# Kernel tuning notes

Measured on AMD Instinct MI355X. Metric: run time of the kernel, lower is better.

The kernel has to match this reference:

```python
import jax, jax.numpy as jnp
import numpy as np

B, S, E, H, M, N_BLOCKS, V = 32, 32, 512, 8, 2, 4, 10000
START = 0

def _pos_encoding(s_len, e_dim):
    # Standard sinusoidal positional encoding (base 10000), as in the repo's PositionalEncoding.
    pos = np.arange(s_len)[:, None].astype(np.float32)
    div = np.exp(np.arange(0, e_dim, 2).astype(np.float32) * (-np.log(10000.0) / e_dim))
    pe = np.zeros((s_len, e_dim), dtype=np.float32)
    pe[:, 0::2] = np.sin(pos * div)
    pe[:, 1::2] = np.cos(pos * div)
    return jnp.asarray(pe)

def _ln(x, g, b, eps=1e-5):
    mu = x.mean(-1, keepdims=True)
    var = ((x - mu) ** 2).mean(-1, keepdims=True)
    return g * (x - mu) / jnp.sqrt(var + eps) + b

def _mha(q_in, kv_in, Wq, Wk, Wv, Wo, bq, bk, bv, bo):
    b_, tq, e = q_in.shape
    dh = e // H
    q = (q_in @ Wq + bq).reshape(b_, tq, H, dh)
    k = (kv_in @ Wk + bk).reshape(b_, -1, H, dh)
    v = (kv_in @ Wv + bv).reshape(b_, -1, H, dh)
    att = jax.nn.softmax(jnp.einsum('bqhd,bkhd->bhqk', q, k) * (1.0 / np.sqrt(dh)), axis=-1)
    out = jnp.einsum('bhqk,bkhd->bqhd', att, v).reshape(b_, tq, e)
    return out @ Wo + bo

def setup_inputs():
    key = jax.random.key(0)
    ks = jax.random.split(key, 8)
    s = 0.02
    return {
        'noise': jax.random.uniform(ks[0], (B, S), dtype=jnp.float32),
        'W_in': jax.random.normal(ks[1], (M, S, S), dtype=jnp.float32) * s,
        'b_in': jnp.zeros((M, S), dtype=jnp.float32),
        'emb': jax.random.normal(ks[2], (V, E), dtype=jnp.float32) * s,
        'Wsa': jax.random.normal(ks[3], (N_BLOCKS, 4, E, E), dtype=jnp.float32) * s,
        'bsa': jnp.zeros((N_BLOCKS, 4, E), dtype=jnp.float32),
        'Wca': jax.random.normal(ks[4], (N_BLOCKS, 4, E, E), dtype=jnp.float32) * s,
        'bca': jnp.zeros((N_BLOCKS, 4, E), dtype=jnp.float32),
        'Wff': jax.random.normal(ks[5], (N_BLOCKS, 2, E, E), dtype=jnp.float32) * s,
        'bff': jnp.zeros((N_BLOCKS, 2, E), dtype=jnp.float32),
        'ln_g': jnp.ones((N_BLOCKS, 3, E), dtype=jnp.float32),
        'ln_b': jnp.zeros((N_BLOCKS, 3, E), dtype=jnp.float32),
        'soft_W': jax.random.normal(ks[6], (E, V), dtype=jnp.float32) * s,
        'soft_b': jnp.zeros((V,), dtype=jnp.float32),
    }

def reference(noise, W_in, b_in, emb, Wsa, bsa, Wca, bca, Wff, bff, ln_g, ln_b, soft_W, soft_b):
    pe = _pos_encoding(S, E)  # [S, E]
    # inEmb2: M stacked Linear(S, S) applied to the latent noise vector
    w = noise
    for m in range(M):
        w = w @ W_in[m] + b_in[m]
    # unsqueeze(-1).repeat(1,1,E): broadcast the scalar per position across the embedding dim
    w = jnp.broadcast_to(w[:, :, None], (B, S, E))
    # <START> token embedding + positional encoding of position 0
    Y = jnp.broadcast_to(emb[START], (B, 1, E)) + pe[0:1]
    out_sent = [jnp.broadcast_to(jax.nn.one_hot(START, V, dtype=jnp.float32), (B, V))]
    for tok in range(1, S):
        output = Y  # [B, tok, E]
        wt = w[:, :tok]
        for n in range(N_BLOCKS):
            h = _ln(output + _mha(output, output, Wsa[n, 0], Wsa[n, 1], Wsa[n, 2], Wsa[n, 3], bsa[n, 0], bsa[n, 1], bsa[n, 2], bsa[n, 3]), ln_g[n, 0], ln_b[n, 0])
            h = _ln(h + _mha(h, wt, Wca[n, 0], Wca[n, 1], Wca[n, 2], Wca[n, 3], bca[n, 0], bca[n, 1], bca[n, 2], bca[n, 3]), ln_g[n, 1], ln_b[n, 1])
            ff = jax.nn.relu(h @ Wff[n, 0] + bff[n, 0]) @ Wff[n, 1] + bff[n, 1]
            output = _ln(h + ff, ln_g[n, 2], ln_b[n, 2])
        out_tok = output[:, tok - 1]                       # [B, E]
        probs = jax.nn.softmax(out_tok @ soft_W + soft_b)  # [B, V]
        out_sent.append(probs)
        ids = jnp.argmax(probs, axis=-1)                   # greedy token
        nxt = emb[ids] + pe[tok]                           # embed + add posenc (Y[:, tok] += posEnc[:, tok])
        Y = jnp.concatenate([Y, nxt[:, None]], axis=1)
    return jnp.stack(out_sent, axis=1)  # [B, S, V]
```

## Files before the change

### kernel.cpp

```cpp
#include <hip/hip_runtime.h>
#include <cmath>

constexpr int kB = 32, kS = 32, kE = 512, kH = 8, kV = 10000, kNB = 4;
constexpr int kQ = 3 * kE;
constexpr int ROWS = 4;
constexpr int TT = 1024;

__device__ float g_w[kB * kS];
__device__ float g_pe[kS * kE];
__device__ float g_Y[kB * kS * kE];
__device__ float g_qkvbuf[kNB][kB * kS * kQ];
__device__ float g_actb[kNB][kB * kS * kE];
__device__ float g_logits[kB * kV];
__device__ float g_U[kNB * kE * kH];
__device__ float g_a0[kNB * kH];
__device__ float g_G[kNB * kH * kE];
__device__ float g_c0[kNB * kE];
__device__ float g_ck[kNB * kE];
__device__ float g_cv[kNB * kE];

__global__ void onehot_k(float* __restrict__ out) {
    int i = blockIdx.x * 256 + threadIdx.x;
    if (i >= kB * kV) return;
    int b = i / kV, v = i - b * kV;
    out[(size_t)b * kS * kV + v] = (v == 0) ? 1.f : 0.f;
}

__global__ void pe_k(float* __restrict__ pe) {
    int i = blockIdx.x * 256 + threadIdx.x;
    int s = i >> 9, e = i & 511;
    int base = e & ~1;
    float div = expf((float)base * (-logf(10000.f) / (float)kE));
    float ang = (float)s * div;
    pe[i] = (e & 1) ? cosf(ang) : sinf(ang);
}

__global__ void compute_w_k(const float* __restrict__ noise, const float* __restrict__ W_in,
                            const float* __restrict__ b_in, float* __restrict__ w) {
    __shared__ float X[kB * kS], T[kB * kS];
    int tid = threadIdx.x;
    X[tid] = noise[tid];
    __syncthreads();
    int r = tid >> 5, c = tid & 31;
    float acc = b_in[c];
    for (int k = 0; k < 32; ++k) acc = fmaf(X[r * 32 + k], W_in[k * 32 + c], acc);
    T[tid] = acc;
    __syncthreads();
    acc = b_in[32 + c];
    for (int k = 0; k < 32; ++k) acc = fmaf(T[r * 32 + k], W_in[1024 + k * 32 + c], acc);
    w[tid] = acc;
}

__global__ __launch_bounds__(256) void initY_k(const float* __restrict__ emb,
                                               const float* __restrict__ pe,
                                               float* __restrict__ Y,
                                               const float* __restrict__ Wq0,
                                               const float* __restrict__ bq0,
                                               float* __restrict__ qkv0) {
    __shared__ float ys[kE];
    int b = blockIdx.x, tid = threadIdx.x;
    for (int j = tid; j < kE; j += 256) {
        float v = emb[j] + pe[j];
        Y[(size_t)(b * kS) * kE + j] = v;
        ys[j] = v;
    }
    __syncthreads();
#pragma unroll
    for (int m = 0; m < 6; ++m) {
        int j = tid + 256 * m;
        const float* Wc = Wq0 + (size_t)(j >> 9) * (kE * kE) + (j & 511);
        float acc = bq0[j];
        for (int k = 0; k < kE; ++k) acc = fmaf(ys[k], Wc[(size_t)k * kE], acc);
        qkv0[(size_t)(b * kS) * kQ + j] = acc;
    }
}

__global__ __launch_bounds__(256) void colsum_k(const float* __restrict__ Wca,
                                                float* __restrict__ ck, float* __restrict__ cv) {
    int n = blockIdx.x, q = blockIdx.y;
    const float* Wk = Wca + (size_t)n * 4 * kE * kE + kE * kE;
    const float* Wv = Wk + kE * kE;
    __shared__ float p1[2][128], p2[2][128];
    int jj = threadIdx.x & 127, half = threadIdx.x >> 7;
    int j = q * 128 + jj;
    float s1 = 0.f, s2 = 0.f;
    for (int e = half * 256; e < half * 256 + 256; ++e) {
        s1 += Wk[(size_t)e * kE + j];
        s2 += Wv[(size_t)e * kE + j];
    }
    p1[half][jj] = s1; p2[half][jj] = s2;
    __syncthreads();
    if (half == 0) {
        ck[n * kE + j] = p1[0][jj] + p1[1][jj];
        cv[n * kE + j] = p2[0][jj] + p2[1][jj];
    }
}

__global__ __launch_bounds__(256) void precross2_k(const float* __restrict__ Wca,
                                                   const float* __restrict__ bca,
                                                   const float* __restrict__ ck,
                                                   const float* __restrict__ cv,
                                                   float* __restrict__ U, float* __restrict__ a0,
                                                   float* __restrict__ G, float* __restrict__ c0) {
    int n = blockIdx.x, s = blockIdx.y;
    const float* Wq = Wca + (size_t)n * 4 * kE * kE;
    const float* Wo = Wq + 3 * kE * kE;
    const float* bq = bca + n * 4 * kE;
    const float* bv = bq + 2 * kE;
    const float* bo = bq + 3 * kE;
    __shared__ float cks[kE], cvs[kE];
    __shared__ float cred[2][128];
    int tid = threadIdx.x;
    for (int p = tid; p < kE; p += 256) { cks[p] = ck[n * kE + p]; cvs[p] = cv[n * kE + p]; }
    __syncthreads();
    for (int p = tid; p < 128 * kH; p += 256) {
        int e = s * 128 + (p >> 3), h = p & 7;
        float acc = 0.f;
        for (int d = 0; d < 64; ++d) acc = fmaf(Wq[(size_t)e * kE + h * 64 + d], cks[h * 64 + d], acc);
        U[n * kE * kH + e * kH + h] = acc;
    }
    for (int p = tid; p < kH * 128; p += 256) {
        int h = p >> 7, j = s * 128 + (p & 127);
        float acc = 0.f;
        for (int d = 0; d < 64; ++d) acc = fmaf(cvs[h * 64 + d], Wo[(size_t)(h * 64 + d) * kE + j], acc);
        G[n * kH * kE + h * kE + j] = acc;
    }
    {
        int jj = tid & 127, half = tid >> 7;
        int j = s * 128 + jj;
        float acc = 0.f;
        for (int e = half * 256; e < half * 256 + 256; ++e) acc = fmaf(bv[e], Wo[(size_t)e * kE + j], acc);
        cred[half][jj] = acc;
        __syncthreads();
        if (half == 0) c0[n * kE + j] = bo[j] + cred[0][jj] + cred[1][jj];
    }
    if (s == 0 && tid < kH) {
        float acc = 0.f;
        for (int d = 0; d < 64; ++d) acc = fmaf(bq[tid * 64 + d], cks[tid * 64 + d], acc);
        a0[n * kH + tid] = acc;
    }
}

__device__ __forceinline__ void rowsum4_1024(float v[ROWS], float (*red)[ROWS], float out[ROWS]) {
    int lane = threadIdx.x & 63, w = threadIdx.x >> 6;
#pragma unroll
    for (int i = 0; i < ROWS; ++i) {
        float s = v[i];
#pragma unroll
        for (int o = 32; o > 0; o >>= 1) s += __shfl_xor(s, o);
        v[i] = s;
    }
    if (lane == 0) {
#pragma unroll
        for (int i = 0; i < ROWS; ++i) red[w][i] = v[i];
    }
    __syncthreads();
#pragma unroll
    for (int i = 0; i < ROWS; ++i) {
        float s = 0.f;
#pragma unroll
        for (int w2 = 0; w2 < 16; ++w2) s += red[w2][i];
        out[i] = s;
    }
    __syncthreads();
}

__device__ __forceinline__ void ln4_1024(float val[ROWS], const float* __restrict__ g,
                                         const float* __restrict__ bb, float (*red)[ROWS], int j,
                                         bool act) {
    float s[ROWS], mean[ROWS], var[ROWS];
#pragma unroll
    for (int i = 0; i < ROWS; ++i) s[i] = act ? val[i] : 0.f;
    rowsum4_1024(s, red, mean);
#pragma unroll
    for (int i = 0; i < ROWS; ++i) {
        mean[i] *= (1.f / (float)kE);
        if (act) val[i] -= mean[i];
        s[i] = act ? val[i] * val[i] : 0.f;
    }
    rowsum4_1024(s, red, var);
#pragma unroll
    for (int i = 0; i < ROWS; ++i) {
        float rstd = rsqrtf(var[i] * (1.f / (float)kE) + 1e-5f);
        if (act) val[i] = g[j] * val[i] * rstd + bb[j];
    }
}

__device__ __forceinline__ void gemm_phase4(const float (*in)[kE], const float* __restrict__ W,
                                            float (*out)[kE], int kg, int jt) {
    float acc[ROWS][4];
#pragma unroll
    for (int i = 0; i < ROWS; ++i)
#pragma unroll
        for (int c = 0; c < 4; ++c) acc[i][c] = 0.f;
    const int kbase = kg * 64;
    const int j4 = jt * 4;
#pragma unroll 8
    for (int kk = 0; kk < 64; kk += 4) {
        float4 av[ROWS];
#pragma unroll
        for (int i = 0; i < ROWS; ++i) av[i] = *(const float4*)(&in[i][kbase + kk]);
        const float* Wr = W + (size_t)(kbase + kk) * kE + j4;
        const float4 w0 = *(const float4*)(Wr);
        const float4 w1 = *(const float4*)(Wr + kE);
        const float4 w2 = *(const float4*)(Wr + 2 * kE);
        const float4 w3 = *(const float4*)(Wr + 3 * kE);
#pragma unroll
        for (int i = 0; i < ROWS; ++i) {
            acc[i][0] = fmaf(av[i].x, w0.x, acc[i][0]);
            acc[i][0] = fmaf(av[i].y, w1.x, acc[i][0]);
            acc[i][0] = fmaf(av[i].z, w2.x, acc[i][0]);
            acc[i][0] = fmaf(av[i].w, w3.x, acc[i][0]);
            acc[i][1] = fmaf(av[i].x, w0.y, acc[i][1]);
            acc[i][1] = fmaf(av[i].y, w1.y, acc[i][1]);
            acc[i][1] = fmaf(av[i].z, w2.y, acc[i][1]);
            acc[i][1] = fmaf(av[i].w, w3.y, acc[i][1]);
            acc[i][2] = fmaf(av[i].x, w0.z, acc[i][2]);
            acc[i][2] = fmaf(av[i].y, w1.z, acc[i][2]);
            acc[i][2] = fmaf(av[i].z, w2.z, acc[i][2]);
            acc[i][2] = fmaf(av[i].w, w3.z, acc[i][2]);
            acc[i][3] = fmaf(av[i].x, w0.w, acc[i][3]);
            acc[i][3] = fmaf(av[i].y, w1.w, acc[i][3]);
            acc[i][3] = fmaf(av[i].z, w2.w, acc[i][3]);
            acc[i][3] = fmaf(av[i].w, w3.w, acc[i][3]);
        }
    }
    if (kg == 0) {
#pragma unroll
        for (int i = 0; i < ROWS; ++i)
            *(float4*)(&out[i][j4]) = make_float4(acc[i][0], acc[i][1], acc[i][2], acc[i][3]);
    }
    __syncthreads();
#pragma unroll
    for (int r = 1; r < 8; ++r) {
        if (kg == r) {
#pragma unroll
            for (int i = 0; i < ROWS; ++i) {
                float4 c = *(float4*)(&out[i][j4]);
                c.x += acc[i][0]; c.y += acc[i][1]; c.z += acc[i][2]; c.w += acc[i][3];
                *(float4*)(&out[i][j4]) = c;
            }
        }
        __syncthreads();
    }
}

__global__ __launch_bounds__(1024) void tail4w_k(
    const float* __restrict__ qkv_cur, const float* __restrict__ in_res,
    const float* __restrict__ Wo, const float* __restrict__ bo,
    const float* __restrict__ g0, const float* __restrict__ lb0,
    const float* __restrict__ Um, const float* __restrict__ a0m,
    const float* __restrict__ Gm, const float* __restrict__ c0m,
    const float* __restrict__ g1, const float* __restrict__ lb1,
    const float* __restrict__ W1, const float* __restrict__ fb1,
    const float* __restrict__ W2, const float* __restrict__ fb2,
    const float* __restrict__ g2, const float* __restrict__ lb2,
    const float* __restrict__ wvec, float* __restrict__ act_out,
    const float* __restrict__ Wqn, const float* __restrict__ bqn,
    float* __restrict__ qkv_next, int t, int r0_off) {
    __shared__ float bufA[ROWS][kE];
    __shared__ float bufC[ROWS][kE];
    __shared__ float Us[kE * kH];
    __shared__ float att_s[16][kS];
    __shared__ float alp[ROWS][kH][4];
    __shared__ float om_s[ROWS][kH];
    __shared__ float w_s[kS];
    __shared__ float red[16][ROWS];

    const int b = blockIdx.x;
    const int r0 = r0_off + blockIdx.y * ROWS;
    const int tid = threadIdx.x;
    const int lane = tid & 63, wid = tid >> 6;
    const int kg = tid >> 7, jt = tid & 127;
    const bool act = (tid < kE);
    int rr[ROWS]; bool valid[ROWS];
#pragma unroll
    for (int i = 0; i < ROWS; ++i) {
        int r = r0 + i;
        valid[i] = (r < t);
        rr[i] = valid[i] ? r : (t - 1);
    }

    for (int p = tid; p < ROWS * kE; p += TT) {
        int i = p >> 9, d = p & 511;
        bufA[i][d] = qkv_cur[(size_t)(b * kS + rr[i]) * kQ + d];
    }
    for (int p = tid; p < kE * kH; p += TT) Us[p] = Um[p];
    if (tid < t) w_s[tid] = wvec[b * kS + tid];
    __syncthreads();

    {
        const int i = wid & 3;
        const int hb = (wid >> 2) * 2;
#pragma unroll
        for (int hh = 0; hh < 2; ++hh) {
            const int h = hb + hh;
            float sc = -3.0e38f;
            if (lane < t) {
                const float* Kr = qkv_cur + (size_t)(b * kS + lane) * kQ + kE + h * 64;
                float a = 0.f;
#pragma unroll
                for (int d4 = 0; d4 < 16; ++d4) {
                    const float4 kv = *(const float4*)(Kr + d4 * 4);
                    const float4 qv = *(const float4*)(&bufA[i][h * 64 + d4 * 4]);
                    a = fmaf(qv.x, kv.x, a); a = fmaf(qv.y, kv.y, a);
                    a = fmaf(qv.z, kv.z, a); a = fmaf(qv.w, kv.w, a);
                }
                sc = a * 0.125f;
            }
            float m = sc;
#pragma unroll
            for (int o = 32; o > 0; o >>= 1) m = fmaxf(m, __shfl_xor(m, o));
            float e = (lane < t) ? expf(sc - m) : 0.f;
            float ss = e;
#pragma unroll
            for (int o = 32; o > 0; o >>= 1) ss += __shfl_xor(ss, o);
            if (lane < t) att_s[wid][lane] = e / ss;
            float acc = 0.f;
            const float* Vb = qkv_cur + (size_t)(b * kS) * kQ + 2 * kE + h * 64 + lane;
            for (int k = 0; k < t; ++k) acc = fmaf(att_s[wid][k], Vb[(size_t)k * kQ], acc);
            bufA[i][h * 64 + lane] = acc;
        }
    }
    __syncthreads();

    float val[ROWS], hreg[ROWS], h2reg[ROWS];

    float resv[ROWS];
#pragma unroll
    for (int i = 0; i < ROWS; ++i)
        resv[i] = act ? in_res[(size_t)(b * kS + rr[i]) * kE + tid] : 0.f;
    gemm_phase4(bufA, Wo, bufC, kg, jt);
    {
        float btid = act ? bo[tid] : 0.f;
#pragma unroll
        for (int i = 0; i < ROWS; ++i) val[i] = act ? (bufC[i][tid] + btid + resv[i]) : 0.f;
        ln4_1024(val, g0, lb0, red, act ? tid : 0, act);
#pragma unroll
        for (int i = 0; i < ROWS; ++i) {
            hreg[i] = val[i];
            if (act) bufA[i][tid] = val[i];
        }
    }
    __syncthreads();

    if (tid < ROWS * kH * 4) {
        int i = tid >> 5, h = (tid >> 2) & 7, cs = tid & 3;
        float a = 0.f;
        for (int e = cs * 128; e < cs * 128 + 128; ++e) a = fmaf(bufA[i][e], Us[e * kH + h], a);
        alp[i][h][cs] = a;
    }
    __syncthreads();
    if (tid < ROWS * kH) {
        int i = tid >> 3, h = tid & 7;
        float a = a0m[h] + alp[i][h][0] + alp[i][h][1] + alp[i][h][2] + alp[i][h][3];
        a *= 0.125f;
        float mm = -3.0e38f;
        for (int s = 0; s < t; ++s) mm = fmaxf(mm, a * w_s[s]);
        float se = 0.f, sw = 0.f;
        for (int s = 0; s < t; ++s) {
            float ex = expf(a * w_s[s] - mm);
            se += ex;
            sw = fmaf(ex, w_s[s], sw);
        }
        om_s[i][h] = sw / se;
    }
    __syncthreads();

    {
        float ctid = act ? c0m[tid] : 0.f;
#pragma unroll
        for (int i = 0; i < ROWS; ++i) {
            float v = ctid + hreg[i];
            if (act) {
#pragma unroll
                for (int h = 0; h < kH; ++h) v = fmaf(om_s[i][h], Gm[h * kE + tid], v);
            }
            val[i] = act ? v : 0.f;
        }
        ln4_1024(val, g1, lb1, red, act ? tid : 0, act);
#pragma unroll
        for (int i = 0; i < ROWS; ++i) {
            h2reg[i] = val[i];
            if (act) bufA[i][tid] = val[i];
        }
    }
    __syncthreads();

    gemm_phase4(bufA, W1, bufC, kg, jt);
    {
        float btid = act ? fb1[tid] : 0.f;
#pragma unroll
        for (int i = 0; i < ROWS; ++i) val[i] = act ? fmaxf(bufC[i][tid] + btid, 0.f) : 0.f;
    }
    __syncthreads();
    {
#pragma unroll
        for (int i = 0; i < ROWS; ++i)
            if (act) bufA[i][tid] = val[i];
    }
    __syncthreads();

    gemm_phase4(bufA, W2, bufC, kg, jt);
    {
        float btid = act ? fb2[tid] : 0.f;
#pragma unroll
        for (int i = 0; i < ROWS; ++i) val[i] = act ? (bufC[i][tid] + btid + h2reg[i]) : 0.f;
        ln4_1024(val, g2, lb2, red, act ? tid : 0, act);
    }
    __syncthreads();
    {
#pragma unroll
        for (int i = 0; i < ROWS; ++i) {
            if (act) {
                if (valid[i]) act_out[(size_t)(b * kS + r0 + i) * kE + tid] = val[i];
                bufA[i][tid] = val[i];
            }
        }
    }
    __syncthreads();

    if (Wqn != nullptr) {
#pragma unroll
        for (int slab = 0; slab < 3; ++slab) {
            gemm_phase4(bufA, Wqn + (size_t)slab * kE * kE, bufC, kg, jt);
            if (act) {
                float bj = bqn[slab * kE + tid];
#pragma unroll
                for (int i = 0; i < ROWS; ++i)
                    if (valid[i])
                        qkv_next[(size_t)(b * kS + r0 + i) * kQ + slab * kE + tid] =
                            bufC[i][tid] + bj;
            }
            __syncthreads();
        }
    }
}

__global__ __launch_bounds__(256) void logits_k(const float* __restrict__ act3,
                                                const float* __restrict__ softW,
                                                const float* __restrict__ softb,
                                                float* __restrict__ logits, int tokm1) {
    __shared__ float xs[kB][kE];
    int tid = threadIdx.x;
    for (int p = tid; p < kB * kE; p += 256) {
        int bb = p >> 9, k = p & 511;
        xs[bb][k] = act3[(size_t)(bb * kS + tokm1) * kE + k];
    }
    __syncthreads();
    const int tx = tid & 31, ty = tid >> 5;
    int j0 = blockIdx.x * 64 + 2 * tx;
    int j0c = (j0 + 1 < kV) ? j0 : (kV - 2);
    float acc[4][2];
#pragma unroll
    for (int r = 0; r < 4; ++r) { acc[r][0] = softb[j0c]; acc[r][1] = softb[j0c + 1]; }
#pragma unroll 8
    for (int k = 0; k < kE; ++k) {
        const float2 wv = *(const float2*)(softW + (size_t)k * kV + j0c);
#pragma unroll
        for (int r = 0; r < 4; ++r) {
            float xv = xs[4 * ty + r][k];
            acc[r][0] = fmaf(xv, wv.x, acc[r][0]);
            acc[r][1] = fmaf(xv, wv.y, acc[r][1]);
        }
    }
    if (j0 + 1 < kV) {
#pragma unroll
        for (int r = 0; r < 4; ++r) {
            logits[(size_t)(4 * ty + r) * kV + j0] = acc[r][0];
            logits[(size_t)(4 * ty + r) * kV + j0 + 1] = acc[r][1];
        }
    } else if (j0 < kV) {
#pragma unroll
        for (int r = 0; r < 4; ++r) logits[(size_t)(4 * ty + r) * kV + j0] = acc[r][0];
    }
}

__global__ __launch_bounds__(256) void softargmax_k(const float* __restrict__ logits,
                                                    float* __restrict__ outp,
                                                    const float* __restrict__ emb,
                                                    const float* __restrict__ pe_t,
                                                    float* __restrict__ Y, int tok) {
    __shared__ float redf[4];
    __shared__ int redi[4];
    int b = blockIdx.x, tid = threadIdx.x;
    const float* lg = logits + (size_t)b * kV;
    float m = -3.4e38f;
    int mi = 0;
    for (int j = tid; j < kV; j += 256) {
        float v = lg[j];
        if (v > m) { m = v; mi = j; }
    }
#pragma unroll
    for (int o = 32; o > 0; o >>= 1) {
        float m2 = __shfl_xor(m, o);
        int i2 = __shfl_xor(mi, o);
        if (m2 > m || (m2 == m && i2 < mi)) { m = m2; mi = i2; }
    }
    int wid = tid >> 6;
    if ((tid & 63) == 0) { redf[wid] = m; redi[wid] = mi; }
    __syncthreads();
    m = redf[0]; mi = redi[0];
#pragma unroll
    for (int wv = 1; wv < 4; ++wv) {
        if (redf[wv] > m || (redf[wv] == m && redi[wv] < mi)) { m = redf[wv]; mi = redi[wv]; }
    }
    __syncthreads();
    float ssum = 0.f;
    for (int j = tid; j < kV; j += 256) ssum += expf(lg[j] - m);
    {
#pragma unroll
        for (int o = 32; o > 0; o >>= 1) ssum += __shfl_xor(ssum, o);
        if ((tid & 63) == 0) redf[wid] = ssum;
        __syncthreads();
        ssum = redf[0] + redf[1] + redf[2] + redf[3];
    }
    float inv = 1.f / ssum;
    float* orow = outp + (size_t)b * ((size_t)kS * kV);
    for (int j = tid; j < kV; j += 256) orow[j] = expf(lg[j] - m) * inv;
    const float* erow = emb + (size_t)mi * kE;
    float* yrow = Y + (size_t)(b * kS + tok) * kE;
    for (int j = tid; j < kE; j += 256) yrow[j] = erow[j] + pe_t[j];
}

__global__ __launch_bounds__(256) void qkvrow_k(const float* __restrict__ Y,
                                                const float* __restrict__ Wq0,
                                                const float* __restrict__ bq0,
                                                float* __restrict__ qkv0, int tok) {
    __shared__ float ys[kB][kE];
    int tid = threadIdx.x;
    for (int p = tid; p < kB * kE; p += 256) {
        int bb = p >> 9, k = p & 511;
        ys[bb][k] = Y[(size_t)(bb * kS + tok) * kE + k];
    }
    __syncthreads();
    const int tx = tid & 63, ty = tid >> 6;
    const int j = blockIdx.x * 64 + tx;
    const float* Wc = Wq0 + (size_t)(j >> 9) * (kE * kE) + (j & 511);
    float acc[8];
    float bj = bq0[j];
#pragma unroll
    for (int i = 0; i < 8; ++i) acc[i] = bj;
#pragma unroll 4
    for (int k = 0; k < kE; k += 4) {
        float w0 = Wc[(size_t)(k + 0) * kE];
        float w1 = Wc[(size_t)(k + 1) * kE];
        float w2 = Wc[(size_t)(k + 2) * kE];
        float w3 = Wc[(size_t)(k + 3) * kE];
#pragma unroll
        for (int i = 0; i < 8; ++i) {
            const float4 yv = *(const float4*)(&ys[ty * 8 + i][k]);
            float a = acc[i];
            a = fmaf(yv.x, w0, a);
            a = fmaf(yv.y, w1, a);
            a = fmaf(yv.z, w2, a);
            a = fmaf(yv.w, w3, a);
            acc[i] = a;
        }
    }
#pragma unroll
    for (int i = 0; i < 8; ++i)
        qkv0[(size_t)((ty * 8 + i) * kS + tok) * kQ + j] = acc[i];
}

extern "C" void kernel_launch(void* const* d_in, const int* in_sizes, int n_in, void* d_out,
                              int out_size, void* d_ws, size_t ws_size, hipStream_t stream) {
    const float* noise = (const float*)d_in[0];
    const float* W_in = (const float*)d_in[1];
    const float* b_in = (const float*)d_in[2];
    const float* emb = (const float*)d_in[3];
    const float* Wsa = (const float*)d_in[4];
    const float* bsa = (const float*)d_in[5];
    const float* Wca = (const float*)d_in[6];
    const float* bca = (const float*)d_in[7];
    const float* Wff = (const float*)d_in[8];
    const float* bff = (const float*)d_in[9];
    const float* ln_g = (const float*)d_in[10];
    const float* ln_b = (const float*)d_in[11];
    const float* softW = (const float*)d_in[12];
    const float* softb = (const float*)d_in[13];
    float* out = (float*)d_out;
    (void)d_ws; (void)ws_size; (void)in_sizes; (void)n_in; (void)out_size;

    float *w_, *pe_, *Y_, *qkvb_, *actb_, *lg_, *U_, *a0_, *G_, *c0_, *ck_, *cv_;
    hipGetSymbolAddress((void**)&w_, HIP_SYMBOL(g_w));
    hipGetSymbolAddress((void**)&pe_, HIP_SYMBOL(g_pe));
    hipGetSymbolAddress((void**)&Y_, HIP_SYMBOL(g_Y));
    hipGetSymbolAddress((void**)&qkvb_, HIP_SYMBOL(g_qkvbuf));
    hipGetSymbolAddress((void**)&actb_, HIP_SYMBOL(g_actb));
    hipGetSymbolAddress((void**)&lg_, HIP_SYMBOL(g_logits));
    hipGetSymbolAddress((void**)&U_, HIP_SYMBOL(g_U));
    hipGetSymbolAddress((void**)&a0_, HIP_SYMBOL(g_a0));
    hipGetSymbolAddress((void**)&G_, HIP_SYMBOL(g_G));
    hipGetSymbolAddress((void**)&c0_, HIP_SYMBOL(g_c0));
    hipGetSymbolAddress((void**)&ck_, HIP_SYMBOL(g_ck));
    hipGetSymbolAddress((void**)&cv_, HIP_SYMBOL(g_cv));

    float* qb[kNB];
    float* ab[kNB];
    for (int n = 0; n < kNB; ++n) {
        qb[n] = qkvb_ + (size_t)n * (kB * kS * kQ);
        ab[n] = actb_ + (size_t)n * (kB * kS * kE);
    }

    dim3 blk(256);
    hipLaunchKernelGGL(onehot_k, dim3((kB * kV + 255) / 256), blk, 0, stream, out);
    hipLaunchKernelGGL(pe_k, dim3(kS * kE / 256), blk, 0, stream, pe_);
    hipLaunchKernelGGL(compute_w_k, dim3(1), dim3(1024), 0, stream, noise, W_in, b_in, w_);
    hipLaunchKernelGGL(initY_k, dim3(kB), blk, 0, stream, emb, pe_, Y_, Wsa, bsa, qb[0]);
    hipLaunchKernelGGL(colsum_k, dim3(kNB, 4), blk, 0, stream, Wca, ck_, cv_);
    hipLaunchKernelGGL(precross2_k, dim3(kNB, 4), blk, 0, stream, Wca, bca, ck_, cv_, U_, a0_,
                       G_, c0_);

    for (int tok = 1; tok < kS; ++tok) {
        const int t = tok;
        const int nch = (t + ROWS - 1) / ROWS;
        for (int n = 0; n < kNB; ++n) {
            const float* in_res = (n == 0) ? Y_ : ab[n - 1];
            const float* Wn = Wsa + (size_t)n * 4 * kE * kE;
            const float* bn = bsa + (size_t)n * 4 * kE;
            const float* Wf = Wff + (size_t)n * 2 * kE * kE;
            const float* bf = bff + (size_t)n * 2 * kE;
            const float* Wqn = (n < 3) ? (Wsa + (size_t)(n + 1) * 4 * kE * kE) : nullptr;
            const float* bqn = (n < 3) ? (bsa + (size_t)(n + 1) * 4 * kE) : bsa;
            float* qnext = (n < 3) ? qb[n + 1] : nullptr;
            const int grid_y = (n == 3) ? 1 : nch;
            const int r0_off = (n == 3) ? ((t > ROWS) ? (t - ROWS) : 0) : 0;
            hipLaunchKernelGGL(tail4w_k, dim3(kB, grid_y), dim3(TT), 0, stream,
                               qb[n], in_res,
                               Wn + 3 * kE * kE, bn + 3 * kE,
                               ln_g + (size_t)(n * 3 + 0) * kE, ln_b + (size_t)(n * 3 + 0) * kE,
                               U_ + n * kE * kH, a0_ + n * kH, G_ + n * kH * kE, c0_ + n * kE,
                               ln_g + (size_t)(n * 3 + 1) * kE, ln_b + (size_t)(n * 3 + 1) * kE,
                               Wf, bf, Wf + kE * kE, bf + kE,
                               ln_g + (size_t)(n * 3 + 2) * kE, ln_b + (size_t)(n * 3 + 2) * kE,
                               w_, ab[n], Wqn, bqn, qnext, t, r0_off);
        }
        hipLaunchKernelGGL(logits_k, dim3(157), blk, 0, stream, ab[3], softW, softb, lg_,
                           tok - 1);
        hipLaunchKernelGGL(softargmax_k, dim3(kB), blk, 0, stream, lg_,
                           out + (size_t)tok * kV, emb, pe_ + (size_t)tok * kE, Y_, tok);
        hipLaunchKernelGGL(qkvrow_k, dim3(24), blk, 0, stream, Y_, Wsa, bsa, qb[0], tok);
    }
}
```

Baseline: 13.32 ms.

## Split next-block QKV projection out of fused tail kernel into tiled GEMM

Removes the fused QKV projection for the next block from the per-(batch,row-chunk) tail kernel and instead launches a separate shared-memory tiled GEMM over all B*t rows. In the fused version each block of 4 rows re-streamed the full 512x1536 weight matrix. The tiled GEMM reuses weight tiles across 32 rows per block. This adds one extra launch per block and a round trip of activations through global memory.

Measured after the change: 15.66 ms. 17.6% more time.

```diff
diff --git a/kernel.cpp b/kernel.cpp
--- a/kernel.cpp
+++ b/kernel.cpp
@@ -255,9 +255,7 @@
     const float* __restrict__ W1, const float* __restrict__ fb1,
     const float* __restrict__ W2, const float* __restrict__ fb2,
     const float* __restrict__ g2, const float* __restrict__ lb2,
-    const float* __restrict__ wvec, float* __restrict__ act_out,
-    const float* __restrict__ Wqn, const float* __restrict__ bqn,
-    float* __restrict__ qkv_next, int t, int r0_off) {
+    const float* __restrict__ wvec, float* __restrict__ act_out, int t, int r0_off) {
     __shared__ float bufA[ROWS][kE];
     __shared__ float bufC[ROWS][kE];
     __shared__ float Us[kE * kH];
@@ -407,32 +405,77 @@
 #pragma unroll
         for (int i = 0; i < ROWS; ++i) val[i] = act ? (bufC[i][tid] + btid + h2reg[i]) : 0.f;
         ln4_1024(val, g2, lb2, red, act ? tid : 0, act);
-    }
-    __syncthreads();
-    {
-#pragma unroll
-        for (int i = 0; i < ROWS; ++i) {
-            if (act) {
-                if (valid[i]) act_out[(size_t)(b * kS + r0 + i) * kE + tid] = val[i];
-                bufA[i][tid] = val[i];
+#pragma unroll
+        for (int i = 0; i < ROWS; ++i)
+            if (act && valid[i]) act_out[(size_t)(b * kS + r0 + i) * kE + tid] = val[i];
+    }
+}
+
+__global__ __launch_bounds__(256) void gemm_k(const float* __restrict__ A,
+                                              const float* __restrict__ W,
+                                              const float* __restrict__ bias,
+                                              float* __restrict__ C, int t, int R, int ncols,
+                                              int w_ld, int grouped, int relu, long out_bs,
+                                              long out_rs) {
+    __shared__ float As[32][33];
+    __shared__ float Ws[32][68];
+    const int tid = threadIdx.x;
+    const int tile_j = blockIdx.x * 64;
+    const int tile_r = blockIdx.y * 32;
+    const float* Wt = W;
+    int jbase = tile_j;
+    if (grouped) { Wt = W + (size_t)(tile_j >> 9) * kE * kE; jbase = tile_j & 511; }
+    const int tx = tid & 15, ty = tid >> 4;
+    float acc[2][4] = {{0.f, 0.f, 0.f, 0.f}, {0.f, 0.f, 0.f, 0.f}};
+    for (int k0 = 0; k0 < kE; k0 += 32) {
+#pragma unroll
+        for (int p = tid; p < 32 * 32; p += 256) {
+            int rr = p >> 5, cc = p & 31;
+            int r = tile_r + rr;
+            float v = 0.f;
+            if (r < R) {
+                int b = r / t, s = r - b * t;
+                v = A[(size_t)(b * kS + s) * kE + k0 + cc];
             }
-        }
-    }
-    __syncthreads();
-
-    if (Wqn != nullptr) {
-#pragma unroll
-        for (int slab = 0; slab < 3; ++slab) {
-            gemm_phase4(bufA, Wqn + (size_t)slab * kE * kE, bufC, kg, jt);
-            if (act) {
-                float bj = bqn[slab * kE + tid];
-#pragma unroll
-                for (int i = 0; i < ROWS; ++i)
-                    if (valid[i])
-                        qkv_next[(size_t)(b * kS + r0 + i) * kQ + slab * kE + tid] =
-                            bufC[i][tid] + bj;
-            }
-            __syncthreads();
+            As[rr][cc] = v;
+        }
+#pragma unroll
+        for (int p = tid; p < 32 * 64; p += 256) {
+            int kk = p >> 6, jj = p & 63;
+            float v = 0.f;
+            if (tile_j + jj < ncols) v = Wt[(size_t)(k0 + kk) * w_ld + jbase + jj];
+            Ws[kk][jj] = v;
+        }
+        __syncthreads();
+#pragma unroll
+        for (int kk = 0; kk < 32; ++kk) {
+            float a0v = As[ty * 2 + 0][kk];
+            float a1v = As[ty * 2 + 1][kk];
+            const float4 wv = *reinterpret_cast<const float4*>(&Ws[kk][tx * 4]);
+            acc[0][0] = fmaf(a0v, wv.x, acc[0][0]);
+            acc[0][1] = fmaf(a0v, wv.y, acc[0][1]);
+            acc[0][2] = fmaf(a0v, wv.z, acc[0][2]);
+            acc[0][3] = fmaf(a0v, wv.w, acc[0][3]);
+            acc[1][0] = fmaf(a1v, wv.x, acc[1][0]);
+            acc[1][1] = fmaf(a1v, wv.y, acc[1][1]);
+            acc[1][2] = fmaf(a1v, wv.z, acc[1][2]);
+            acc[1][3] = fmaf(a1v, wv.w, acc[1][3]);
+        }
+        __syncthreads();
+    }
+#pragma unroll
+    for (int i = 0; i < 2; ++i) {
+        int r = tile_r + ty * 2 + i;
+        if (r >= R) continue;
+        int b = r / t, s = r - b * t;
+        float* Crow = C + (size_t)b * out_bs + (size_t)s * out_rs;
+#pragma unroll
+        for (int q = 0; q < 4; ++q) {
+            int j = tile_j + tx * 4 + q;
+            if (j >= ncols) continue;
+            float v = acc[i][q] + bias[j];
+            if (relu) v = fmaxf(v, 0.f);
+            Crow[j] = v;
         }
     }
 }
@@ -614,6 +657,7 @@
 
     for (int tok = 1; tok < kS; ++tok) {
         const int t = tok;
+        const int R = kB * t;
         const int nch = (t + ROWS - 1) / ROWS;
         for (int n = 0; n < kNB; ++n) {
             const float* in_res = (n == 0) ? Y_ : ab[n - 1];
@@ -621,9 +665,6 @@
             const float* bn = bsa + (size_t)n * 4 * kE;
             const float* Wf = Wff + (size_t)n * 2 * kE * kE;
             const float* bf = bff + (size_t)n * 2 * kE;
-            const float* Wqn = (n < 3) ? (Wsa + (size_t)(n + 1) * 4 * kE * kE) : nullptr;
-            const float* bqn = (n < 3) ? (bsa + (size_t)(n + 1) * 4 * kE) : bsa;
-            float* qnext = (n < 3) ? qb[n + 1] : nullptr;
             const int grid_y = (n == 3) ? 1 : nch;
             const int r0_off = (n == 3) ? ((t > ROWS) ? (t - ROWS) : 0) : 0;
             hipLaunchKernelGGL(tail4w_k, dim3(kB, grid_y), dim3(TT), 0, stream,
@@ -634,7 +675,13 @@
                                ln_g + (size_t)(n * 3 + 1) * kE, ln_b + (size_t)(n * 3 + 1) * kE,
                                Wf, bf, Wf + kE * kE, bf + kE,
                                ln_g + (size_t)(n * 3 + 2) * kE, ln_b + (size_t)(n * 3 + 2) * kE,
-                               w_, ab[n], Wqn, bqn, qnext, t, r0_off);
+                               w_, ab[n], t, r0_off);
+            if (n < 3) {
+                hipLaunchKernelGGL(gemm_k, dim3(24, (R + 31) / 32), blk, 0, stream, ab[n],
+                                   Wsa + (size_t)(n + 1) * 4 * kE * kE,
+                                   bsa + (size_t)(n + 1) * 4 * kE, qb[n + 1], t, R, kQ, kE, 1, 0,
+                                   (long)(kS * kQ), (long)kQ);
+            }
         }
         hipLaunchKernelGGL(logits_k, dim3(157), blk, 0, stream, ab[3], softW, softb, lg_,
                            tok - 1);
```

## Stage GEMM weight chunks into LDS via async global_load_lds double buffering

Applied to the files above, without the earlier changes.

Replaces direct global float4 weight loads in the fused tail kernel's GEMM phases with a double-buffered LDS staging pipeline. It uses __builtin_amdgcn_global_load_lds to prefetch 2-row-per-k-group weight chunks while computing on the previous chunk. The aim is to overlap weight fetch latency with FMA work. In exchange it adds 32 KB of shared memory and a __syncthreads per chunk (32 per GEMM), which may cut occupancy. There is also a risk of missing waits on the async LDS loads.

Measured after the change: 19.19 ms. +44.1%, slower.

```diff
diff --git a/kernel.cpp b/kernel.cpp
--- a/kernel.cpp
+++ b/kernel.cpp
@@ -5,6 +5,9 @@
 constexpr int kQ = 3 * kE;
 constexpr int ROWS = 4;
 constexpr int TT = 1024;
+
+#define GLD_SRC const __attribute__((address_space(1))) void*
+#define GLD_DST __attribute__((address_space(3))) void*
 
 __device__ float g_w[kB * kS];
 __device__ float g_pe[kS * kE];
@@ -186,43 +189,43 @@
     }
 }
 
-__device__ __forceinline__ void gemm_phase4(const float (*in)[kE], const float* __restrict__ W,
-                                            float (*out)[kE], int kg, int jt) {
-    float acc[ROWS][4];
-#pragma unroll
-    for (int i = 0; i < ROWS; ++i)
-#pragma unroll
-        for (int c = 0; c < 4; ++c) acc[i][c] = 0.f;
+__device__ __forceinline__ void stage_chunk(const float* __restrict__ W, float* __restrict__ Wb,
+                                            int c, int tid) {
+#pragma unroll
+    for (int l = 0; l < 2; ++l) {
+        const int g = (tid >> 8) + (l << 2);
+        const int r = (tid >> 7) & 1;
+        const int col = (tid & 127) << 2;
+        const float* src = W + (size_t)((g << 6) + (c << 1) + r) * kE + col;
+        float* dst = Wb + ((tid >> 6) << 8) + (l << 12);
+        __builtin_amdgcn_global_load_lds((GLD_SRC)src, (GLD_DST)dst, 16, 0, 0);
+    }
+}
+
+__device__ __forceinline__ void gemm_phase_st(const float (*in)[kE], const float* __restrict__ W,
+                                              float (*out)[kE], float* __restrict__ Wst,
+                                              int kg, int jt, int tid) {
+    float acc[ROWS][4] = {};
     const int kbase = kg * 64;
     const int j4 = jt * 4;
-#pragma unroll 8
-    for (int kk = 0; kk < 64; kk += 4) {
-        float4 av[ROWS];
-#pragma unroll
-        for (int i = 0; i < ROWS; ++i) av[i] = *(const float4*)(&in[i][kbase + kk]);
-        const float* Wr = W + (size_t)(kbase + kk) * kE + j4;
-        const float4 w0 = *(const float4*)(Wr);
-        const float4 w1 = *(const float4*)(Wr + kE);
-        const float4 w2 = *(const float4*)(Wr + 2 * kE);
-        const float4 w3 = *(const float4*)(Wr + 3 * kE);
+    stage_chunk(W, Wst, 0, tid);
+    for (int c = 0; c < 32; ++c) {
+        __syncthreads();
+        if (c < 31) stage_chunk(W, Wst + ((c + 1) & 1) * 4096, c + 1, tid);
+        const float* Wb = Wst + (c & 1) * 4096 + (kg << 1) * kE + j4;
+        const float4 w0 = *(const float4*)(Wb);
+        const float4 w1 = *(const float4*)(Wb + kE);
 #pragma unroll
         for (int i = 0; i < ROWS; ++i) {
-            acc[i][0] = fmaf(av[i].x, w0.x, acc[i][0]);
-            acc[i][0] = fmaf(av[i].y, w1.x, acc[i][0]);
-            acc[i][0] = fmaf(av[i].z, w2.x, acc[i][0]);
-            acc[i][0] = fmaf(av[i].w, w3.x, acc[i][0]);
-            acc[i][1] = fmaf(av[i].x, w0.y, acc[i][1]);
-            acc[i][1] = fmaf(av[i].y, w1.y, acc[i][1]);
-            acc[i][1] = fmaf(av[i].z, w2.y, acc[i][1]);
-            acc[i][1] = fmaf(av[i].w, w3.y, acc[i][1]);
-            acc[i][2] = fmaf(av[i].x, w0.z, acc[i][2]);
-            acc[i][2] = fmaf(av[i].y, w1.z, acc[i][2]);
-            acc[i][2] = fmaf(av[i].z, w2.z, acc[i][2]);
-            acc[i][2] = fmaf(av[i].w, w3.z, acc[i][2]);
-            acc[i][3] = fmaf(av[i].x, w0.w, acc[i][3]);
-            acc[i][3] = fmaf(av[i].y, w1.w, acc[i][3]);
-            acc[i][3] = fmaf(av[i].z, w2.w, acc[i][3]);
-            acc[i][3] = fmaf(av[i].w, w3.w, acc[i][3]);
+            const float2 av = *(const float2*)(&in[i][kbase + (c << 1)]);
+            acc[i][0] = fmaf(av.x, w0.x, acc[i][0]);
+            acc[i][0] = fmaf(av.y, w1.x, acc[i][0]);
+            acc[i][1] = fmaf(av.x, w0.y, acc[i][1]);
+            acc[i][1] = fmaf(av.y, w1.y, acc[i][1]);
+            acc[i][2] = fmaf(av.x, w0.z, acc[i][2]);
+            acc[i][2] = fmaf(av.y, w1.z, acc[i][2]);
+            acc[i][3] = fmaf(av.x, w0.w, acc[i][3]);
+            acc[i][3] = fmaf(av.y, w1.w, acc[i][3]);
         }
     }
     if (kg == 0) {
@@ -236,9 +239,9 @@
         if (kg == r) {
 #pragma unroll
             for (int i = 0; i < ROWS; ++i) {
-                float4 c = *(float4*)(&out[i][j4]);
-                c.x += acc[i][0]; c.y += acc[i][1]; c.z += acc[i][2]; c.w += acc[i][3];
-                *(float4*)(&out[i][j4]) = c;
+                float4 c2 = *(float4*)(&out[i][j4]);
+                c2.x += acc[i][0]; c2.y += acc[i][1]; c2.z += acc[i][2]; c2.w += acc[i][3];
+                *(float4*)(&out[i][j4]) = c2;
             }
         }
         __syncthreads();
@@ -261,6 +264,7 @@
     __shared__ float bufA[ROWS][kE];
     __shared__ float bufC[ROWS][kE];
     __shared__ float Us[kE * kH];
+    __shared__ float Wst[2][4096];
     __shared__ float att_s[16][kS];
     __shared__ float alp[ROWS][kH][4];
     __shared__ float om_s[ROWS][kH];
@@ -273,6 +277,7 @@
     const int lane = tid & 63, wid = tid >> 6;
     const int kg = tid >> 7, jt = tid & 127;
     const bool act = (tid < kE);
+    float* Wstp = &Wst[0][0];
     int rr[ROWS]; bool valid[ROWS];
 #pragma unroll
     for (int i = 0; i < ROWS; ++i) {
@@ -330,7 +335,7 @@
 #pragma unroll
     for (int i = 0; i < ROWS; ++i)
         resv[i] = act ? in_res[(size_t)(b * kS + rr[i]) * kE + tid] : 0.f;
-    gemm_phase4(bufA, Wo, bufC, kg, jt);
+    gemm_phase_st(bufA, Wo, bufC, Wstp, kg, jt, tid);
     {
         float btid = act ? bo[tid] : 0.f;
 #pragma unroll
@@ -387,7 +392,7 @@
     }
     __syncthreads();
 
-    gemm_phase4(bufA, W1, bufC, kg, jt);
+    gemm_phase_st(bufA, W1, bufC, Wstp, kg, jt, tid);
     {
         float btid = act ? fb1[tid] : 0.f;
 #pragma unroll
@@ -401,7 +406,7 @@
     }
     __syncthreads();
 
-    gemm_phase4(bufA, W2, bufC, kg, jt);
+    gemm_phase_st(bufA, W2, bufC, Wstp, kg, jt, tid);
     {
         float btid = act ? fb2[tid] : 0.f;
 #pragma unroll
@@ -423,7 +428,7 @@
     if (Wqn != nullptr) {
 #pragma unroll
         for (int slab = 0; slab < 3; ++slab) {
-            gemm_phase4(bufA, Wqn + (size_t)slab * kE * kE, bufC, kg, jt);
+            gemm_phase_st(bufA, Wqn + (size_t)slab * kE * kE, bufC, Wstp, kg, jt, tid);
             if (act) {
                 float bj = bqn[slab * kE + tid];
 #pragma unroll
```
